# Kernel tuning notes

Measured on AMD Instinct MI355X. Metric: run time of the kernel, lower is better.

## Reference

```python
import jax, jax.numpy as jnp
import numpy as np

NUM_HEADS = 16


def setup_inputs() -> dict:
    key = jax.random.key(0)
    ks = jax.random.split(key, 6)
    B, S, D = 2, 2048, 1024
    x = jax.random.normal(ks[0], (B, S, D), dtype=jnp.float32)
    # Linear weights stored as [d_in, d_out] so forward is x @ W (qkv_bias=False)
    scale = 1.0 / np.sqrt(D)
    Wq = jax.random.normal(ks[1], (D, D), dtype=jnp.float32) * scale
    Wk = jax.random.normal(ks[2], (D, D), dtype=jnp.float32) * scale
    Wv = jax.random.normal(ks[3], (D, D), dtype=jnp.float32) * scale
    Wo = jax.random.normal(ks[4], (D, D), dtype=jnp.float32) * scale
    bo = jax.random.normal(ks[5], (D,), dtype=jnp.float32) * 0.01
    return {"x": x, "Wq": Wq, "Wk": Wk, "Wv": Wv, "Wo": Wo, "bo": bo}


def reference(x, Wq, Wk, Wv, Wo, bo):
    B, S, D = x.shape
    H = NUM_HEADS
    hd = D // H

    def split_heads(t):  # [B,S,D] -> [B,H,S,hd]
        return t.reshape(B, S, H, hd).transpose(0, 2, 1, 3)

    q = split_heads(x @ Wq)
    k = split_heads(x @ Wk)
    v = split_heads(x @ Wv)

    # full score matrix [B,H,S,S]
    scores = jnp.einsum('bhsd,bhtd->bhst', q, k)
    causal = jnp.triu(jnp.ones((S, S), dtype=bool), k=1)
    scores = jnp.where(causal, -jnp.inf, scores)
    attn = jax.nn.softmax(scores * (hd ** -0.5), axis=-1)
    # dropout p=0.0 -> identity
    out = jnp.einsum('bhst,bhtd->bhsd', attn, v)
    out = out.transpose(0, 2, 1, 3).reshape(B, S, D)
    return out @ Wo + bo
```

## Files before the change

kernel.cpp:

```cpp
#include <hip/hip_runtime.h>

typedef unsigned short ushort_t;
typedef unsigned int uint_t;
typedef __attribute__((ext_vector_type(8))) short short8;
typedef __attribute__((ext_vector_type(4))) float floatx4;

#define S_LEN 2048
#define D_DIM 1024
#define H_NUM 16
#define HD 64
#define GBUF (128 * 32)

__device__ __forceinline__ float bf2f(ushort_t u) {
    union { uint_t i; float f; } c; c.i = ((uint_t)u) << 16; return c.f;
}
__device__ __forceinline__ ushort_t f2bf(float f) {
    union { float f; uint_t i; } c; c.f = f;
    uint_t r = c.i + 0x7fffu + ((c.i >> 16) & 1u);
    return (ushort_t)(r >> 16);
}

__device__ __forceinline__ void g2l16(const ushort_t* g, ushort_t* l) {
    __builtin_amdgcn_global_load_lds(
        (const __attribute__((address_space(1))) void*)g,
        (__attribute__((address_space(3))) void*)l, 16, 0, 0);
}

__global__ __launch_bounds__(256, 4) void cast_x_kernel(
        const float* __restrict__ in, ushort_t* __restrict__ out) {
    const int idx = (blockIdx.x * 256 + threadIdx.x) * 4;
    const float4 v = *(const float4*)(in + idx);
    ushort4 o;
    o.x = f2bf(v.x); o.y = f2bf(v.y); o.z = f2bf(v.z); o.w = f2bf(v.w);
    *(ushort4*)(out + idx) = o;
}

__global__ __launch_bounds__(256, 2) void transpose4_kernel(
        const float* __restrict__ W0, const float* __restrict__ W1,
        const float* __restrict__ W2, const float* __restrict__ W3,
        ushort_t* __restrict__ T0, ushort_t* __restrict__ T1,
        ushort_t* __restrict__ T2, ushort_t* __restrict__ T3) {
    const int z = blockIdx.z;
    const float* in  = (z == 0) ? W0 : (z == 1) ? W1 : (z == 2) ? W2 : W3;
    ushort_t*    out = (z == 0) ? T0 : (z == 1) ? T1 : (z == 2) ? T2 : T3;
    __shared__ __align__(16) ushort_t t[64][65];
    const int r0 = blockIdx.y * 64, c0 = blockIdx.x * 64;
    const int tr = threadIdx.x >> 4;
    const int tc = (threadIdx.x & 15) * 4;
#pragma unroll
    for (int i = 0; i < 4; ++i) {
        const int row = tr + i * 16;
        const float4 v = *(const float4*)(in + (size_t)(r0 + row) * D_DIM + c0 + tc);
        t[row][tc + 0] = f2bf(v.x); t[row][tc + 1] = f2bf(v.y);
        t[row][tc + 2] = f2bf(v.z); t[row][tc + 3] = f2bf(v.w);
    }
    __syncthreads();
#pragma unroll
    for (int i = 0; i < 4; ++i) {
        const int n = tr + i * 16;
        ushort4 v;
        v.x = t[tc + 0][n]; v.y = t[tc + 1][n];
        v.z = t[tc + 2][n]; v.w = t[tc + 3][n];
        *(ushort4*)(out + (size_t)(c0 + n) * D_DIM + r0 + tc) = v;
    }
}

__device__ __forceinline__ void gemm_tile(
        const ushort_t* __restrict__ A, const ushort_t* __restrict__ BT,
        const int m0, const int n0,
        ushort_t* As, ushort_t* Bs, floatx4 acc[4][4]) {
    const int tid  = threadIdx.x;
    const int w    = tid >> 6;
    const int wm   = (w >> 1) * 64;
    const int wn   = (w & 1) * 64;
    const int lrow = tid & 15;
    const int kq   = ((tid & 63) >> 4) * 8;

    const int flat0 = tid * 8;
    const int flat1 = (256 + tid) * 8;
    const int row0 = flat0 >> 5, kk0 = flat0 & 31;
    const int row1 = flat1 >> 5, kk1 = flat1 & 31;

    const ushort_t* ga0 = A  + (size_t)(m0 + row0) * D_DIM + kk0;
    const ushort_t* gb0 = BT + (size_t)(n0 + row0) * D_DIM + kk0;
    const ushort_t* ga1 = A  + (size_t)(m0 + row1) * D_DIM + kk1;
    const ushort_t* gb1 = BT + (size_t)(n0 + row1) * D_DIM + kk1;

    g2l16(ga0, As + flat0);
    g2l16(gb0, Bs + flat0);
    g2l16(ga1, As + flat1);
    g2l16(gb1, Bs + flat1);
    asm volatile("s_waitcnt vmcnt(0)" ::: "memory");
    __syncthreads();

    int cur = 0;
    for (int k0 = 0; k0 < D_DIM; k0 += 32) {
        const ushort_t* Ac = As + cur * GBUF;
        const ushort_t* Bc = Bs + cur * GBUF;
        short8 av[4], bv[4];
#pragma unroll
        for (int i = 0; i < 4; ++i)
            av[i] = *(const short8*)(Ac + (wm + i * 16 + lrow) * 32 + kq);
#pragma unroll
        for (int j = 0; j < 4; ++j)
            bv[j] = *(const short8*)(Bc + (wn + j * 16 + lrow) * 32 + kq);

        if (k0 + 32 < D_DIM) {
            ushort_t* An = As + (cur ^ 1) * GBUF;
            ushort_t* Bn = Bs + (cur ^ 1) * GBUF;
            g2l16(ga0 + k0 + 32, An + flat0);
            g2l16(gb0 + k0 + 32, Bn + flat0);
            g2l16(ga1 + k0 + 32, An + flat1);
            g2l16(gb1 + k0 + 32, Bn + flat1);
        }

#pragma unroll
        for (int i = 0; i < 4; ++i)
#pragma unroll
            for (int j = 0; j < 4; ++j)
                acc[i][j] = __builtin_amdgcn_mfma_f32_16x16x32_bf16(
                    av[i], bv[j], acc[i][j], 0, 0, 0);

        asm volatile("s_waitcnt vmcnt(0)" ::: "memory");
        __syncthreads();
        cur ^= 1;
    }
}

__global__ __launch_bounds__(256, 3) void gemm_qkv_kernel(
        const ushort_t* __restrict__ A,
        const ushort_t* __restrict__ WqT, const ushort_t* __restrict__ WkT,
        const ushort_t* __restrict__ WvT,
        ushort_t* __restrict__ Qo, ushort_t* __restrict__ Ko,
        ushort_t* __restrict__ Vo) {
    const ushort_t* BT = (blockIdx.z == 0) ? WqT : (blockIdx.z == 1) ? WkT : WvT;
    ushort_t* C        = (blockIdx.z == 0) ? Qo  : (blockIdx.z == 1) ? Ko  : Vo;
    const float sc     = (blockIdx.z == 0) ? 0.18033688f : 1.0f;
    __shared__ __align__(16) ushort_t As[2 * GBUF];
    __shared__ __align__(16) ushort_t Bs[2 * GBUF];
    const int m0 = blockIdx.y * 128, n0 = blockIdx.x * 128;

    floatx4 acc[4][4] = {};
    gemm_tile(A, BT, m0, n0, As, Bs, acc);

    const int tid = threadIdx.x;
    const int w = tid >> 6, wm = (w >> 1) * 64, wn = (w & 1) * 64;
    const int lrow = tid & 15;
    const int rquad = ((tid & 63) >> 4) * 4;
#pragma unroll
    for (int i = 0; i < 4; ++i) {
        const int mbase = m0 + wm + i * 16 + rquad;
#pragma unroll
        for (int j = 0; j < 4; ++j) {
            const int gn = n0 + wn + j * 16 + lrow;
#pragma unroll
            for (int r = 0; r < 4; ++r)
                C[(size_t)(mbase + r) * D_DIM + gn] = f2bf(acc[i][j][r] * sc);
        }
    }
}

__global__ __launch_bounds__(256, 2) void gemm_out_kernel(
        const ushort_t* __restrict__ A, const ushort_t* __restrict__ WoT,
        const float* __restrict__ bias, float* __restrict__ C) {
    __shared__ __align__(16) ushort_t As[2 * GBUF];
    __shared__ __align__(16) ushort_t Bs[2 * GBUF];
    const int m0 = blockIdx.y * 128, n0 = blockIdx.x * 128;

    floatx4 acc[4][4] = {};
    gemm_tile(A, WoT, m0, n0, As, Bs, acc);

    const int tid = threadIdx.x;
    const int w = tid >> 6, wm = (w >> 1) * 64, wn = (w & 1) * 64;
    const int lrow = tid & 15;
    const int rquad = ((tid & 63) >> 4) * 4;
#pragma unroll
    for (int i = 0; i < 4; ++i) {
        const int mbase = m0 + wm + i * 16 + rquad;
#pragma unroll
        for (int j = 0; j < 4; ++j) {
            const int gn = n0 + wn + j * 16 + lrow;
            const float badd = bias[gn];
#pragma unroll
            for (int r = 0; r < 4; ++r)
                C[(size_t)(mbase + r) * D_DIM + gn] = acc[i][j][r] + badd;
        }
    }
}

__global__ __launch_bounds__(256, 4) void attn_mfma_kernel(
        const ushort_t* __restrict__ Q, const ushort_t* __restrict__ K,
        const ushort_t* __restrict__ V, ushort_t* __restrict__ O) {
    __shared__ __align__(16) ushort_t Ks[64 * 64];
    __shared__ __align__(16) ushort_t Vt[64 * 64];
    __shared__ __align__(16) ushort_t Ps[4][16 * 64];

    const int bh  = blockIdx.x;
    const int b   = bh >> 4, h = bh & 15;
    const int g   = blockIdx.y & 7;
    const int p   = blockIdx.y >> 3;
    const int qt  = (p == 0) ? g : (p == 1) ? (15 - g)
                  : (p == 2) ? (16 + g) : (31 - g);
    const int q0  = qt * 64;
    const int tid = threadIdx.x;
    const int wq  = tid >> 6;
    const int lane = tid & 63;
    const int col  = lane & 15;
    const int quad = lane >> 4;
    const int c7 = col & 7;
    const int qw0  = q0 + wq * 16;
    const size_t rowbase = (size_t)b * S_LEN;
    const int ch0 = h * HD;

    const int skey = tid >> 2;
    const int schk = tid & 3;
    const int vkp = tid & 31;
    const int vdc = tid >> 5;

    short8 aq[2];
#pragma unroll
    for (int kc = 0; kc < 2; ++kc)
        aq[kc] = *(const short8*)(Q + (rowbase + qw0 + col) * D_DIM
                                    + ch0 + kc * 32 + quad * 8);

    floatx4 oacc[4] = {};
    float mrun[4], lrun[4];
#pragma unroll
    for (int r = 0; r < 4; ++r) { mrun[r] = -1e30f; lrun[r] = 0.0f; }

    const int ntiles = qt + 1;

    short8 krA, krB, vrA, vrB;
    {
        const ushort_t* kg = K + (rowbase + skey) * D_DIM + ch0 + schk * 16;
        krA = *(const short8*)(kg);
        krB = *(const short8*)(kg + 8);
        const ushort_t* vg = V + (rowbase + 2 * vkp) * D_DIM + ch0 + vdc * 8;
        vrA = *(const short8*)(vg);
        vrB = *(const short8*)(vg + D_DIM);
    }

    for (int t = 0; t < ntiles; ++t) {
        const int kb = t * 64;
        __syncthreads();
        {
            const int sw = skey & 7;
            *(short8*)(Ks + skey * 64 + (((2 * schk) ^ sw) << 3)) = krA;
            *(short8*)(Ks + skey * 64 + (((2 * schk + 1) ^ sw) << 3)) = krB;
        }
#pragma unroll
        for (int e = 0; e < 8; ++e) {
            const int d = vdc * 8 + e;
            const uint_t pk = (uint_t)(ushort_t)vrA[e] | ((uint_t)(ushort_t)vrB[e] << 16);
            *(uint_t*)(Vt + d * 64 + ((2 * vkp) ^ ((d & 7) << 3))) = pk;
        }
        {
            const int kbn = (t + 1 < ntiles) ? (t + 1) * 64 : 0;
            const ushort_t* kg = K + (rowbase + kbn + skey) * D_DIM + ch0 + schk * 16;
            krA = *(const short8*)(kg);
            krB = *(const short8*)(kg + 8);
            const ushort_t* vg = V + (rowbase + kbn + 2 * vkp) * D_DIM + ch0 + vdc * 8;
            vrA = *(const short8*)(vg);
            vrB = *(const short8*)(vg + D_DIM);
        }
        __syncthreads();

        if (kb <= qw0 + 15) {
            floatx4 sa[4] = {};
            __builtin_amdgcn_s_setprio(1);
#pragma unroll
            for (int kc = 0; kc < 2; ++kc)
#pragma unroll
                for (int j = 0; j < 4; ++j) {
                    const short8 bk = *(const short8*)(
                        Ks + (j * 16 + col) * 64 + (((kc * 4 + quad) ^ c7) << 3));
                    sa[j] = __builtin_amdgcn_mfma_f32_16x16x32_bf16(
                        aq[kc], bk, sa[j], 0, 0, 0);
                }
            __builtin_amdgcn_s_setprio(0);

            const bool needmask = (kb + 63 > qw0);
            if (needmask) {
#pragma unroll
                for (int j = 0; j < 4; ++j)
#pragma unroll
                    for (int r = 0; r < 4; ++r) {
                        const int row = qw0 + quad * 4 + r;
                        const int key = kb + j * 16 + col;
                        if (key > row) sa[j][r] = -1e30f;
                    }
            }
#pragma unroll
            for (int r = 0; r < 4; ++r) {
                float mx = fmaxf(fmaxf(sa[0][r], sa[1][r]),
                                 fmaxf(sa[2][r], sa[3][r]));
                mx = fmaxf(mx, __shfl_xor(mx, 1));
                mx = fmaxf(mx, __shfl_xor(mx, 2));
                mx = fmaxf(mx, __shfl_xor(mx, 4));
                mx = fmaxf(mx, __shfl_xor(mx, 8));
                const float mn = fmaxf(mrun[r], mx);
                const float al = __builtin_amdgcn_exp2f(mrun[r] - mn);
                mrun[r] = mn;
                float rs = 0.0f;
#pragma unroll
                for (int j = 0; j < 4; ++j) {
                    const float p2 = __builtin_amdgcn_exp2f(sa[j][r] - mn);
                    sa[j][r] = p2;
                    rs += p2;
                }
                lrun[r] = lrun[r] * al + rs;
#pragma unroll
                for (int jd = 0; jd < 4; ++jd) oacc[jd][r] *= al;
            }
            {
                ushort_t* pw = Ps[wq];
#pragma unroll
                for (int j = 0; j < 4; ++j)
#pragma unroll
                    for (int r = 0; r < 4; ++r) {
                        const int row = quad * 4 + r;
                        pw[row * 64 + ((j * 16 + col) ^ ((row & 7) << 3))] =
                            f2bf(sa[j][r]);
                    }
            }
            asm volatile("s_waitcnt lgkmcnt(0)" ::: "memory");
            __builtin_amdgcn_s_setprio(1);
#pragma unroll
            for (int kc = 0; kc < 2; ++kc) {
                const short8 ap = *(const short8*)(
                    Ps[wq] + col * 64 + (((kc * 4 + quad) ^ c7) << 3));
#pragma unroll
                for (int jd = 0; jd < 4; ++jd) {
                    const short8 bv = *(const short8*)(
                        Vt + (jd * 16 + col) * 64 + (((kc * 4 + quad) ^ c7) << 3));
                    oacc[jd] = __builtin_amdgcn_mfma_f32_16x16x32_bf16(
                        ap, bv, oacc[jd], 0, 0, 0);
                }
            }
            __builtin_amdgcn_s_setprio(0);
        }
    }

#pragma unroll
    for (int r = 0; r < 4; ++r) {
        float l = lrun[r];
        l += __shfl_xor(l, 1);
        l += __shfl_xor(l, 2);
        l += __shfl_xor(l, 4);
        l += __shfl_xor(l, 8);
        const int row = qw0 + quad * 4 + r;
        const float inv = 1.0f / l;
#pragma unroll
        for (int jd = 0; jd < 4; ++jd)
            O[(rowbase + row) * D_DIM + ch0 + jd * 16 + col] =
                f2bf(oacc[jd][r] * inv);
    }
}

extern "C" void kernel_launch(void* const* d_in, const int* in_sizes, int n_in,
                              void* d_out, int out_size, void* d_ws, size_t ws_size,
                              hipStream_t stream) {
    const float* x  = (const float*)d_in[0];
    const float* Wq = (const float*)d_in[1];
    const float* Wk = (const float*)d_in[2];
    const float* Wv = (const float*)d_in[3];
    const float* Wo = (const float*)d_in[4];
    const float* bo = (const float*)d_in[5];
    float* out = (float*)d_out;

    char* ws = (char*)d_ws;
    const size_t MB = 1024 * 1024;
    ushort_t* xb  = (ushort_t*)(ws + 0 * MB);
    ushort_t* WqT = (ushort_t*)(ws + 8 * MB);
    ushort_t* WkT = (ushort_t*)(ws + 10 * MB);
    ushort_t* WvT = (ushort_t*)(ws + 12 * MB);
    ushort_t* WoT = (ushort_t*)(ws + 14 * MB);
    ushort_t* Qb  = (ushort_t*)(ws + 16 * MB);
    ushort_t* Kb  = (ushort_t*)(ws + 24 * MB);
    ushort_t* Vb  = (ushort_t*)(ws + 32 * MB);
    ushort_t* Ob  = (ushort_t*)(ws + 40 * MB);

    cast_x_kernel<<<4096, 256, 0, stream>>>(x, xb);
    transpose4_kernel<<<dim3(16, 16, 4), 256, 0, stream>>>(
        Wq, Wk, Wv, Wo, WqT, WkT, WvT, WoT);

    gemm_qkv_kernel<<<dim3(8, 32, 3), 256, 0, stream>>>(
        xb, WqT, WkT, WvT, Qb, Kb, Vb);

    attn_mfma_kernel<<<dim3(32, 32), 256, 0, stream>>>(Qb, Kb, Vb, Ob);

    gemm_out_kernel<<<dim3(8, 32), 256, 0, stream>>>(Ob, WoT, bo, out);
}
```

Before: 198.7 us.

## Halve attention query tile to 32 rows with 2 waves; swap GEMM grid order

The attention kernel now uses 128-thread blocks covering 32 query rows each, with a grid of 64 query tiles per head. K/V staging is redistributed so each thread loads and stores twice as much, and the causal tile count is adjusted. This aims for finer-grained causal load balancing and more blocks in flight, at the cost of re-streaming K/V for every 32 query rows instead of every 64. The GEMM kernels swap which block index walks M versus N, changing block launch order and therefore L2 reuse of the A and weight tiles.

```diff
diff --git a/kernel.cpp b/kernel.cpp
--- a/kernel.cpp
+++ b/kernel.cpp
@@ -138,7 +138,7 @@
     const float sc     = (blockIdx.z == 0) ? 0.18033688f : 1.0f;
     __shared__ __align__(16) ushort_t As[2 * GBUF];
     __shared__ __align__(16) ushort_t Bs[2 * GBUF];
-    const int m0 = blockIdx.y * 128, n0 = blockIdx.x * 128;
+    const int m0 = blockIdx.x * 128, n0 = blockIdx.y * 128;
 
     floatx4 acc[4][4] = {};
     gemm_tile(A, BT, m0, n0, As, Bs, acc);
@@ -165,7 +165,7 @@
         const float* __restrict__ bias, float* __restrict__ C) {
     __shared__ __align__(16) ushort_t As[2 * GBUF];
     __shared__ __align__(16) ushort_t Bs[2 * GBUF];
-    const int m0 = blockIdx.y * 128, n0 = blockIdx.x * 128;
+    const int m0 = blockIdx.x * 128, n0 = blockIdx.y * 128;
 
     floatx4 acc[4][4] = {};
     gemm_tile(A, WoT, m0, n0, As, Bs, acc);
@@ -188,20 +188,19 @@
     }
 }
 
-__global__ __launch_bounds__(256, 4) void attn_mfma_kernel(
+__global__ __launch_bounds__(128, 4) void attn_mfma_kernel(
         const ushort_t* __restrict__ Q, const ushort_t* __restrict__ K,
         const ushort_t* __restrict__ V, ushort_t* __restrict__ O) {
     __shared__ __align__(16) ushort_t Ks[64 * 64];
     __shared__ __align__(16) ushort_t Vt[64 * 64];
-    __shared__ __align__(16) ushort_t Ps[4][16 * 64];
+    __shared__ __align__(16) ushort_t Ps[2][16 * 64];
 
     const int bh  = blockIdx.x;
     const int b   = bh >> 4, h = bh & 15;
     const int g   = blockIdx.y & 7;
     const int p   = blockIdx.y >> 3;
-    const int qt  = (p == 0) ? g : (p == 1) ? (15 - g)
-                  : (p == 2) ? (16 + g) : (31 - g);
-    const int q0  = qt * 64;
+    const int qt  = (p & 1) ? (8 * p + 7 - g) : (8 * p + g);
+    const int q0  = qt * 32;
     const int tid = threadIdx.x;
     const int wq  = tid >> 6;
     const int lane = tid & 63;
@@ -212,10 +211,10 @@
     const size_t rowbase = (size_t)b * S_LEN;
     const int ch0 = h * HD;
 
-    const int skey = tid >> 2;
-    const int schk = tid & 3;
-    const int vkp = tid & 31;
-    const int vdc = tid >> 5;
+    const int skey = tid >> 1;
+    const int sgb  = (tid & 1) * 4;
+    const int vkp  = tid & 31;
+    const int vdcb = (tid >> 5) * 2;
 
     short8 aq[2];
 #pragma unroll
@@ -228,16 +227,18 @@
 #pragma unroll
     for (int r = 0; r < 4; ++r) { mrun[r] = -1e30f; lrun[r] = 0.0f; }
 
-    const int ntiles = qt + 1;
-
-    short8 krA, krB, vrA, vrB;
+    const int ntiles = (q0 + 31) / 64 + 1;
+
+    short8 kr[4], vA[2], vB[2];
     {
-        const ushort_t* kg = K + (rowbase + skey) * D_DIM + ch0 + schk * 16;
-        krA = *(const short8*)(kg);
-        krB = *(const short8*)(kg + 8);
-        const ushort_t* vg = V + (rowbase + 2 * vkp) * D_DIM + ch0 + vdc * 8;
-        vrA = *(const short8*)(vg);
-        vrB = *(const short8*)(vg + D_DIM);
+        const ushort_t* kg = K + (rowbase + skey) * D_DIM + ch0 + sgb * 8;
+#pragma unroll
+        for (int i = 0; i < 4; ++i) kr[i] = *(const short8*)(kg + i * 8);
+        const ushort_t* vg = V + (rowbase + 2 * vkp) * D_DIM + ch0 + vdcb * 8;
+        vA[0] = *(const short8*)(vg);
+        vA[1] = *(const short8*)(vg + 8);
+        vB[0] = *(const short8*)(vg + D_DIM);
+        vB[1] = *(const short8*)(vg + D_DIM + 8);
     }
 
     for (int t = 0; t < ntiles; ++t) {
@@ -245,23 +246,27 @@
         __syncthreads();
         {
             const int sw = skey & 7;
-            *(short8*)(Ks + skey * 64 + (((2 * schk) ^ sw) << 3)) = krA;
-            *(short8*)(Ks + skey * 64 + (((2 * schk + 1) ^ sw) << 3)) = krB;
-        }
-#pragma unroll
-        for (int e = 0; e < 8; ++e) {
-            const int d = vdc * 8 + e;
-            const uint_t pk = (uint_t)(ushort_t)vrA[e] | ((uint_t)(ushort_t)vrB[e] << 16);
-            *(uint_t*)(Vt + d * 64 + ((2 * vkp) ^ ((d & 7) << 3))) = pk;
+#pragma unroll
+            for (int i = 0; i < 4; ++i)
+                *(short8*)(Ks + skey * 64 + (((sgb + i) ^ sw) << 3)) = kr[i];
+        }
+#pragma unroll
+        for (int e = 0; e < 16; ++e) {
+            const int d = vdcb * 8 + e;
+            const uint_t lo = (uint_t)(ushort_t)vA[e >> 3][e & 7];
+            const uint_t hi = (uint_t)(ushort_t)vB[e >> 3][e & 7];
+            *(uint_t*)(Vt + d * 64 + ((2 * vkp) ^ ((d & 7) << 3))) = lo | (hi << 16);
         }
         {
             const int kbn = (t + 1 < ntiles) ? (t + 1) * 64 : 0;
-            const ushort_t* kg = K + (rowbase + kbn + skey) * D_DIM + ch0 + schk * 16;
-            krA = *(const short8*)(kg);
-            krB = *(const short8*)(kg + 8);
-            const ushort_t* vg = V + (rowbase + kbn + 2 * vkp) * D_DIM + ch0 + vdc * 8;
-            vrA = *(const short8*)(vg);
-            vrB = *(const short8*)(vg + D_DIM);
+            const ushort_t* kg = K + (rowbase + kbn + skey) * D_DIM + ch0 + sgb * 8;
+#pragma unroll
+            for (int i = 0; i < 4; ++i) kr[i] = *(const short8*)(kg + i * 8);
+            const ushort_t* vg = V + (rowbase + kbn + 2 * vkp) * D_DIM + ch0 + vdcb * 8;
+            vA[0] = *(const short8*)(vg);
+            vA[1] = *(const short8*)(vg + 8);
+            vB[0] = *(const short8*)(vg + D_DIM);
+            vB[1] = *(const short8*)(vg + D_DIM + 8);
         }
         __syncthreads();
 
@@ -384,10 +389,10 @@
     transpose4_kernel<<<dim3(16, 16, 4), 256, 0, stream>>>(
         Wq, Wk, Wv, Wo, WqT, WkT, WvT, WoT);
 
-    gemm_qkv_kernel<<<dim3(8, 32, 3), 256, 0, stream>>>(
+    gemm_qkv_kernel<<<dim3(32, 8, 3), 256, 0, stream>>>(
         xb, WqT, WkT, WvT, Qb, Kb, Vb);
 
-    attn_mfma_kernel<<<dim3(32, 32), 256, 0, stream>>>(Qb, Kb, Vb, Ob);
-
-    gemm_out_kernel<<<dim3(8, 32), 256, 0, stream>>>(Ob, WoT, bo, out);
-}
+    attn_mfma_kernel<<<dim3(32, 64), 128, 0, stream>>>(Qb, Kb, Vb, Ob);
+
+    gemm_out_kernel<<<dim3(32, 8), 256, 0, stream>>>(Ob, WoT, bo, out);
+}
```

New measurement: 277.7 us. +39.8%, slower.

## Triple-buffer GEMM LDS tiles with prefetch distance two and partial vmcnt waits

Applied to the files above, without the earlier changes.

The shared GEMM tile routine moves from double to triple LDS buffering and issues global-to-LDS loads two k-steps ahead. It waits with vmcnt(4) so the most recent prefetch can stay in flight, and places one barrier at the top of each iteration instead of a full drain at the end. This aims to hide global load latency behind the MFMA work in the QKV and output projection GEMMs. LDS use per block rises from 32KB to 48KB, which may lower occupancy.

```diff
diff --git a/kernel.cpp b/kernel.cpp
--- a/kernel.cpp
+++ b/kernel.cpp
@@ -86,15 +86,26 @@
     const ushort_t* ga1 = A  + (size_t)(m0 + row1) * D_DIM + kk1;
     const ushort_t* gb1 = BT + (size_t)(n0 + row1) * D_DIM + kk1;
 
+    const int nsteps = D_DIM / 32;
+
     g2l16(ga0, As + flat0);
     g2l16(gb0, Bs + flat0);
     g2l16(ga1, As + flat1);
     g2l16(gb1, Bs + flat1);
-    asm volatile("s_waitcnt vmcnt(0)" ::: "memory");
-    __syncthreads();
+    g2l16(ga0 + 32, As + GBUF + flat0);
+    g2l16(gb0 + 32, Bs + GBUF + flat0);
+    g2l16(ga1 + 32, As + GBUF + flat1);
+    g2l16(gb1 + 32, Bs + GBUF + flat1);
 
     int cur = 0;
-    for (int k0 = 0; k0 < D_DIM; k0 += 32) {
+    for (int k = 0; k < nsteps; ++k) {
+        if (k == nsteps - 1)
+            asm volatile("s_waitcnt vmcnt(0) lgkmcnt(0)" ::: "memory");
+        else
+            asm volatile("s_waitcnt vmcnt(4) lgkmcnt(0)" ::: "memory");
+        __builtin_amdgcn_sched_barrier(0);
+        __builtin_amdgcn_s_barrier();
+
         const ushort_t* Ac = As + cur * GBUF;
         const ushort_t* Bc = Bs + cur * GBUF;
         short8 av[4], bv[4];
@@ -105,13 +116,15 @@
         for (int j = 0; j < 4; ++j)
             bv[j] = *(const short8*)(Bc + (wn + j * 16 + lrow) * 32 + kq);
 
-        if (k0 + 32 < D_DIM) {
-            ushort_t* An = As + (cur ^ 1) * GBUF;
-            ushort_t* Bn = Bs + (cur ^ 1) * GBUF;
-            g2l16(ga0 + k0 + 32, An + flat0);
-            g2l16(gb0 + k0 + 32, Bn + flat0);
-            g2l16(ga1 + k0 + 32, An + flat1);
-            g2l16(gb1 + k0 + 32, Bn + flat1);
+        if (k + 2 < nsteps) {
+            const int nb = (cur + 2 >= 3) ? cur - 1 : cur + 2;
+            ushort_t* An = As + nb * GBUF;
+            ushort_t* Bn = Bs + nb * GBUF;
+            const int ko = (k + 2) * 32;
+            g2l16(ga0 + ko, An + flat0);
+            g2l16(gb0 + ko, Bn + flat0);
+            g2l16(ga1 + ko, An + flat1);
+            g2l16(gb1 + ko, Bn + flat1);
         }
 
 #pragma unroll
@@ -121,9 +134,7 @@
                 acc[i][j] = __builtin_amdgcn_mfma_f32_16x16x32_bf16(
                     av[i], bv[j], acc[i][j], 0, 0, 0);
 
-        asm volatile("s_waitcnt vmcnt(0)" ::: "memory");
-        __syncthreads();
-        cur ^= 1;
+        cur = (cur + 1 >= 3) ? 0 : cur + 1;
     }
 }
 
@@ -136,8 +147,8 @@
     const ushort_t* BT = (blockIdx.z == 0) ? WqT : (blockIdx.z == 1) ? WkT : WvT;
     ushort_t* C        = (blockIdx.z == 0) ? Qo  : (blockIdx.z == 1) ? Ko  : Vo;
     const float sc     = (blockIdx.z == 0) ? 0.18033688f : 1.0f;
-    __shared__ __align__(16) ushort_t As[2 * GBUF];
-    __shared__ __align__(16) ushort_t Bs[2 * GBUF];
+    __shared__ __align__(16) ushort_t As[3 * GBUF];
+    __shared__ __align__(16) ushort_t Bs[3 * GBUF];
     const int m0 = blockIdx.y * 128, n0 = blockIdx.x * 128;
 
     floatx4 acc[4][4] = {};
@@ -163,8 +174,8 @@
 __global__ __launch_bounds__(256, 2) void gemm_out_kernel(
         const ushort_t* __restrict__ A, const ushort_t* __restrict__ WoT,
         const float* __restrict__ bias, float* __restrict__ C) {
-    __shared__ __align__(16) ushort_t As[2 * GBUF];
-    __shared__ __align__(16) ushort_t Bs[2 * GBUF];
+    __shared__ __align__(16) ushort_t As[3 * GBUF];
+    __shared__ __align__(16) ushort_t Bs[3 * GBUF];
     const int m0 = blockIdx.y * 128, n0 = blockIdx.x * 128;
 
     floatx4 acc[4][4] = {};
```

Measured after the change: 194.8 us. 1.02x faster.
